# Kernel optimization log

Measured on AMD Instinct MI355X. Metric: run time of the kernel, lower is better.

## Reference

```python
import jax, jax.numpy as jnp
import numpy as np

B, T, D, H, HH, E = 32, 512, 512, 1024, 128, 4


def _ln(v, g, b, eps=1e-5):
    m = jnp.mean(v, -1, keepdims=True)
    var = jnp.mean((v - m) ** 2, -1, keepdims=True)
    return (v - m) * jax.lax.rsqrt(var + eps) * g + b


def setup_inputs() -> dict:
    key = jax.random.key(0)
    ks = jax.random.split(key, 32)
    n = lambda i, shape, s: jax.random.normal(ks[i], shape, jnp.float32) * s
    inp = {
        "x": n(0, (B, T, D), 1.0),
        # main LSTM weight, stored [in, out] = [D+H, 4H] (torch W.weight.T)
        "Wm": n(1, (D + H, 4 * H), 0.02),
        # hyper-LSTM gate weights [in, out]
        "Wi_h": n(2, (HH, HH), 0.05), "Wi_x": n(3, (D, HH), 0.02), "bi": jnp.zeros(HH),
        "Wg_h": n(4, (HH, HH), 0.05), "Wg_x": n(5, (D, HH), 0.02), "bg": jnp.zeros(HH),
        "Wf_h": n(6, (HH, HH), 0.05), "Wf_x": n(7, (D, HH), 0.02), "bf": jnp.zeros(HH),
        "Wo_h": n(8, (HH, HH), 0.05), "Wo_x": n(9, (D, HH), 0.02), "bo": jnp.zeros(HH),
        # hyper layernorm params
        "lni_g": jnp.ones(HH), "lni_b": jnp.zeros(HH),
        "lng_g": jnp.ones(HH), "lng_b": jnp.zeros(HH),
        "lnf_g": jnp.ones(HH), "lnf_b": jnp.zeros(HH),
        "lno_g": jnp.ones(HH), "lno_b": jnp.zeros(HH),
        "lnc_g": jnp.ones(HH), "lnc_b": jnp.zeros(HH),
        # z projections: [HH, 4E] + bias [4E]
        "pzx_w": n(10, (HH, 4 * E), 0.05), "pzx_b": jnp.zeros(4 * E),
        "pzh_w": n(11, (HH, 4 * E), 0.05), "pzh_b": jnp.zeros(4 * E),
        "pzb_w": n(12, (HH, 4 * E), 0.05), "pzb_b": jnp.zeros(4 * E),
        # d projections: [E, H]; bias projection has its own bias [H]
        "pdx_w": n(13, (E, H), 0.1),
        "pdh_w": n(14, (E, H), 0.1),
        "pb_w": n(15, (E, H), 0.1), "pb_b": jnp.zeros(H),
    }
    return inp


def reference(x, Wm, Wi_h, Wi_x, bi, Wg_h, Wg_x, bg, Wf_h, Wf_x, bf,
              Wo_h, Wo_x, bo, lni_g, lni_b, lng_g, lng_b, lnf_g, lnf_b,
              lno_g, lno_b, lnc_g, lnc_b, pzx_w, pzx_b, pzh_w, pzh_b,
              pzb_w, pzb_b, pdx_w, pdh_w, pb_w, pb_b):
    def step(carry, x_t):
        h, c, hh, ch = carry
        # hyper LSTM cell (with layernorms on pre-activations)
        it = jax.nn.sigmoid(_ln(hh @ Wi_h + x_t @ Wi_x + bi, lni_g, lni_b))
        gt = jnp.tanh(_ln(hh @ Wg_h + x_t @ Wg_x + bg, lng_g, lng_b))
        ft = jax.nn.sigmoid(_ln(hh @ Wf_h + x_t @ Wf_x + bf, lnf_g, lnf_b))
        ot = jax.nn.sigmoid(_ln(hh @ Wo_h + x_t @ Wo_x + bo, lno_g, lno_b))
        ch_new = ft * ch + it * gt
        hh_new = ot * jnp.tanh(_ln(ch_new, lnc_g, lnc_b))
        # embedding vectors z (chunked into 4 gates) -> per-gate scale vectors
        zx = (hh_new @ pzx_w + pzx_b).reshape(-1, 4, E)
        zh = (hh_new @ pzh_w + pzh_b).reshape(-1, 4, E)
        zb = (hh_new @ pzb_w + pzb_b).reshape(-1, 4, E)
        dx = jnp.einsum('bke,eh->bkh', zx, pdx_w).reshape(-1, 4 * H)
        dh = jnp.einsum('bke,eh->bkh', zh, pdh_w).reshape(-1, 4 * H)
        bd = (jnp.einsum('bke,eh->bkh', zb, pb_w) + pb_b).reshape(-1, 4 * H)
        # main LSTM with hyper-scaled gates
        W_x = x_t @ Wm[:D]   # [B, 4H]
        W_h = h @ Wm[D:]     # [B, 4H]
        gates = W_x * dx + W_h * dh + bd
        i, f, o, g = jnp.split(gates, 4, axis=-1)
        c_new = jax.nn.sigmoid(f) * c + jax.nn.sigmoid(i) * jnp.tanh(g)
        h_new = jax.nn.sigmoid(o) * jnp.tanh(c_new)
        return (h_new, c_new, hh_new, ch_new), h_new

    init = (jnp.zeros((B, H), x.dtype), jnp.zeros((B, H), x.dtype),
            jnp.zeros((B, HH), x.dtype), jnp.zeros((B, HH), x.dtype))
    xs = jnp.swapaxes(x, 0, 1)  # [T, B, D]
    (h, c, _, _), ys = jax.lax.scan(step, init, xs)
    outputs = jnp.swapaxes(ys, 0, 1)  # [B, T, H]
    return outputs, h, c
```

## Files before the change

kernel.cpp:

```cpp
#include <hip/hip_runtime.h>
#include <cstdint>
#include <cstddef>

#define NB 32
#define NT 512
#define ND 512
#define NH 1024
#define NC4 4608

typedef short sh8 __attribute__((ext_vector_type(8)));
typedef float f4  __attribute__((ext_vector_type(4)));
typedef unsigned int u4 __attribute__((ext_vector_type(4)));

__device__ __forceinline__ unsigned short f2bf(float x) {
  union { float f; unsigned u; } v; v.f = x;
  unsigned r = v.u + 0x7FFFu + ((v.u >> 16) & 1u);
  return (unsigned short)(r >> 16);
}
__device__ __forceinline__ float bf2f(unsigned short b) {
  union { unsigned u; float f; } v; v.u = ((unsigned)b) << 16; return v.f;
}
__device__ __forceinline__ float blo(unsigned w) { union { unsigned u; float f; } v; v.u = w << 16; return v.f; }
__device__ __forceinline__ float bhi(unsigned w) { union { unsigned u; float f; } v; v.u = w & 0xFFFF0000u; return v.f; }

#define LD16(dst, base, OFFSTR)                                         \
  asm volatile("global_load_dwordx4 %0, %1, off offset:" OFFSTR " sc0 sc1" \
               : "=v"(dst) : "v"(base))

__global__ __launch_bounds__(256) void k_prep(
    const float* __restrict__ wih, const float* __restrict__ wgh,
    const float* __restrict__ wfh, const float* __restrict__ woh,
    const float* __restrict__ pzx, const float* __restrict__ pzh,
    const float* __restrict__ pzb,
    unsigned short* __restrict__ whht, float* __restrict__ pzt,
    unsigned int* __restrict__ hbuf32, int* __restrict__ flags)
{
  int idx = blockIdx.x * 256 + threadIdx.x;
  if (idx < 65536) {
    int g = idx >> 14, r = idx & 16383, j = r >> 7, k = r & 127;
    const float* w = (g == 0) ? wih : (g == 1) ? wgh : (g == 2) ? wfh : woh;
    whht[idx] = f2bf(w[k * 128 + j]);
  }
  if (idx < 6144) {
    int r = idx & 2047, c = r >> 7, k = r & 127;
    int kind = idx >> 11;
    const float* p = (kind == 0) ? pzx : (kind == 1) ? pzh : pzb;
    pzt[idx] = p[k * 16 + c];
    (void)c; (void)k;
  }
  if (idx < 16384)
    __hip_atomic_store(hbuf32 + idx, 0u, __ATOMIC_RELAXED, __HIP_MEMORY_SCOPE_AGENT);
  if (idx < 96)
    __hip_atomic_store(flags + idx, 0, __ATOMIC_RELAXED, __HIP_MEMORY_SCOPE_AGENT);
}

__global__ __launch_bounds__(256) void k_twcat(
    const float* __restrict__ wm, const float* __restrict__ wix,
    const float* __restrict__ wgx, const float* __restrict__ wfx,
    const float* __restrict__ wox, unsigned short* __restrict__ dst)
{
  __shared__ float tile[32][33];
  int bx = blockIdx.x % 144, by = blockIdx.x / 144;
  int n0 = bx * 32, k0 = by * 32;
  int tx = threadIdx.x & 31, ty = threadIdx.x >> 5;
  #pragma unroll
  for (int i = 0; i < 4; i++) {
    int k = k0 + ty + i * 8, n = n0 + tx;
    float v;
    if (n < 4096) v = wm[(size_t)k * 4096 + n];
    else {
      int nn = n - 4096, g = nn >> 7, j = nn & 127;
      const float* w = (g == 0) ? wix : (g == 1) ? wgx : (g == 2) ? wfx : wox;
      v = w[k * 128 + j];
    }
    tile[ty + i * 8][tx] = v;
  }
  __syncthreads();
  #pragma unroll
  for (int i = 0; i < 4; i++)
    dst[(size_t)(n0 + ty + i * 8) * 512 + k0 + tx] = f2bf(tile[tx][ty + i * 8]);
}

__global__ __launch_bounds__(256) void k_twmh(
    const float* __restrict__ wm, unsigned short* __restrict__ dst)
{
  __shared__ float tile[32][33];
  int bx = blockIdx.x % 128, by = blockIdx.x / 128;
  int n0 = bx * 32, k0 = by * 32;
  int tx = threadIdx.x & 31, ty = threadIdx.x >> 5;
  #pragma unroll
  for (int i = 0; i < 4; i++)
    tile[ty + i * 8][tx] = wm[(size_t)(512 + k0 + ty + i * 8) * 4096 + n0 + tx];
  __syncthreads();
  #pragma unroll
  for (int i = 0; i < 4; i++)
    dst[(size_t)(n0 + ty + i * 8) * 1024 + k0 + tx] = f2bf(tile[tx][ty + i * 8]);
}

__global__ __launch_bounds__(256) void k_gemm(
    const float* __restrict__ x, const unsigned short* __restrict__ wt,
    unsigned short* __restrict__ preall)
{
  __shared__ unsigned short la[4096];
  __shared__ unsigned short lb[4096];
  int bid = blockIdx.x;
  int mb = bid % 128, nb = bid / 128;
  int m0 = mb * 128, n0 = nb * 128;
  int tid = threadIdx.x;
  int lane = tid & 63, wid = tid >> 6;
  int wr = (wid >> 1) * 64, wc = (wid & 1) * 64;
  f4 acc[4][4] = {};
  for (int kt = 0; kt < 16; kt++) {
    int k0 = kt * 32;
    __syncthreads();
    {
      int r = tid >> 1, kh = (tid & 1) * 16;
      const float4* srcA = (const float4*)(x + (size_t)(m0 + r) * 512 + k0 + kh);
      unsigned pk[8];
      #pragma unroll
      for (int q = 0; q < 4; q++) {
        float4 f = srcA[q];
        pk[q * 2]     = (unsigned)f2bf(f.x) | ((unsigned)f2bf(f.y) << 16);
        pk[q * 2 + 1] = (unsigned)f2bf(f.z) | ((unsigned)f2bf(f.w) << 16);
      }
      int base = r * 64 + kh * 2;
      u4 v0 = {pk[0], pk[1], pk[2], pk[3]}, v1 = {pk[4], pk[5], pk[6], pk[7]};
      *(u4*)((char*)la + ((base)      ^ ((r & 7) << 4))) = v0;
      *(u4*)((char*)la + ((base + 16) ^ ((r & 7) << 4))) = v1;
    }
    {
      int r = tid >> 1, kh = (tid & 1) * 16;
      const u4* srcB = (const u4*)(wt + (size_t)(n0 + r) * 512 + k0 + kh);
      u4 v0 = srcB[0], v1 = srcB[1];
      int base = r * 64 + kh * 2;
      *(u4*)((char*)lb + ((base)      ^ ((r & 7) << 4))) = v0;
      *(u4*)((char*)lb + ((base + 16) ^ ((r & 7) << 4))) = v1;
    }
    __syncthreads();
    int fo = (lane >> 4) * 16;
    sh8 af[4], bfr[4];
    #pragma unroll
    for (int mt = 0; mt < 4; mt++) {
      int r = wr + mt * 16 + (lane & 15);
      af[mt] = *(sh8*)((char*)la + ((r * 64 + fo) ^ ((r & 7) << 4)));
    }
    #pragma unroll
    for (int nt = 0; nt < 4; nt++) {
      int r = wc + nt * 16 + (lane & 15);
      bfr[nt] = *(sh8*)((char*)lb + ((r * 64 + fo) ^ ((r & 7) << 4)));
    }
    #pragma unroll
    for (int mt = 0; mt < 4; mt++)
      #pragma unroll
      for (int nt = 0; nt < 4; nt++)
        acc[mt][nt] = __builtin_amdgcn_mfma_f32_16x16x32_bf16(af[mt], bfr[nt], acc[mt][nt], 0, 0, 0);
  }
  #pragma unroll
  for (int mt = 0; mt < 4; mt++)
    #pragma unroll
    for (int nt = 0; nt < 4; nt++) {
      f4 a = acc[mt][nt];
      #pragma unroll
      for (int rr = 0; rr < 4; rr++) {
        int m = m0 + wr + mt * 16 + (lane >> 4) * 4 + rr;
        int n = n0 + wc + nt * 16 + (lane & 15);
        int b = m >> 9, t = m & 511;
        int nn;
        if (n < 4096) { int g = n >> 10, jh = n & 1023; nn = (jh >> 4) * 64 + g * 16 + (jh & 15); }
        else nn = n;
        preall[(size_t)(t * 32 + b) * NC4 + nn] = f2bf(a[rr]);
      }
    }
}

__global__ __launch_bounds__(256, 1) void k_rec(
    const unsigned short* __restrict__ preall,
    const unsigned short* __restrict__ wmht,
    const unsigned short* __restrict__ whht,
    const float* __restrict__ pzt,
    float* __restrict__ zbuf,
    const float* __restrict__ pdx, const float* __restrict__ pdh,
    const float* __restrict__ pbw, const float* __restrict__ pbb,
    const float* __restrict__ bi, const float* __restrict__ bg,
    const float* __restrict__ bff, const float* __restrict__ bo,
    const float* __restrict__ lnig, const float* __restrict__ lnib,
    const float* __restrict__ lngg, const float* __restrict__ lngb,
    const float* __restrict__ lnfg, const float* __restrict__ lnfb,
    const float* __restrict__ lnog, const float* __restrict__ lnob,
    const float* __restrict__ lncg, const float* __restrict__ lncb,
    const float* __restrict__ pzxb, const float* __restrict__ pzhb,
    const float* __restrict__ pzbb,
    unsigned int* __restrict__ hbuf32,
    float* __restrict__ out,
    int* __restrict__ flags)
{
  __shared__ __align__(16) unsigned short wlds[64 * 1024];
  __shared__ float red[2][32][68];
  __shared__ __align__(16) float zl[32 * 48];
  __shared__ float clds[512];
  __shared__ __align__(16) unsigned wxl[32][32];
  __shared__ float pdl[3][4][16];
  __shared__ float pbbl[16];

  const int tid = threadIdx.x;
  const int lane = tid & 63, wid = tid >> 6;

  if (blockIdx.x >= 64) {
    float* const hyp  = (float*)wlds;
    float* const pzl  = hyp;
    float* const hhs  = hyp + 6400;
    float* const chs  = hyp + 6528;
    float* const actl = hyp + 6656;
    float* const rwav = hyp + 7168;
    float* const redc = hyp + 7184;

    const int b = blockIdx.x - 64;
    const int j = tid & 127, gp = tid >> 7;
    const int ga = gp, gb = gp + 2;

    u4 wa[16], wb[16];
    {
      const u4* s = (const u4*)(whht + (size_t)(ga * 128 + j) * 128);
      #pragma unroll
      for (int i = 0; i < 16; i++) wa[i] = s[i];
      const u4* s2 = (const u4*)(whht + (size_t)(gb * 128 + j) * 128);
      #pragma unroll
      for (int i = 0; i < 16; i++) wb[i] = s2[i];
    }
    for (int i = tid; i < 6144; i += 256)
      pzl[(i >> 7) * 132 + (i & 127)] = pzt[i];

    const float* bias_p[4] = {bi, bg, bff, bo};
    const float* lng_p[4]  = {lnig, lngg, lnfg, lnog};
    const float* lnb_p[4]  = {lnib, lngb, lnfb, lnob};
    float bias_a = bias_p[ga][j], bias_b = bias_p[gb][j];
    float lgam_a = lng_p[ga][j],  lbet_a = lnb_p[ga][j];
    float lgam_b = lng_p[gb][j],  lbet_b = lnb_p[gb][j];
    float lcg = 0.f, lcb = 0.f;
    if (tid < 128) { lcg = lncg[j]; lcb = lncb[j]; hhs[j] = 0.f; chs[j] = 0.f; }
    float zbias = 0.f;
    if (tid < 48) {
      int kind = tid >> 4, c = tid & 15;
      zbias = ((kind == 0) ? pzxb : (kind == 1) ? pzhb : pzbb)[c];
    }
    __syncthreads();

    const f4* h4 = (const f4*)hhs;
    for (int t = 0; t < NT; t++) {
      float xa = bf2f(preall[(size_t)(t * 32 + b) * NC4 + 4096 + ga * 128 + j]);
      float xb = bf2f(preall[(size_t)(t * 32 + b) * NC4 + 4096 + gb * 128 + j]);
      float sa = bias_a, sb = bias_b;
      #pragma unroll
      for (int i = 0; i < 16; i++) {
        f4 h0 = h4[2 * i], h1 = h4[2 * i + 1];
        u4 w = wa[i];
        sa += blo(w.x) * h0[0] + bhi(w.x) * h0[1] + blo(w.y) * h0[2] + bhi(w.y) * h0[3]
            + blo(w.z) * h1[0] + bhi(w.z) * h1[1] + blo(w.w) * h1[2] + bhi(w.w) * h1[3];
        w = wb[i];
        sb += blo(w.x) * h0[0] + bhi(w.x) * h0[1] + blo(w.y) * h0[2] + bhi(w.y) * h0[3]
            + blo(w.z) * h1[0] + bhi(w.z) * h1[1] + blo(w.w) * h1[2] + bhi(w.w) * h1[3];
      }
      sa += xa; sb += xb;
      float a1 = sa, a2 = sa * sa, b1 = sb, b2 = sb * sb;
      #pragma unroll
      for (int m = 1; m < 64; m <<= 1) {
        a1 += __shfl_xor(a1, m); a2 += __shfl_xor(a2, m);
        b1 += __shfl_xor(b1, m); b2 += __shfl_xor(b2, m);
      }
      if ((tid & 63) == 0) {
        int w = tid >> 6;
        rwav[w * 4] = a1; rwav[w * 4 + 1] = a2; rwav[w * 4 + 2] = b1; rwav[w * 4 + 3] = b2;
      }
      __syncthreads();
      int w0 = gp * 2, w1 = gp * 2 + 1;
      float sum_a = rwav[w0 * 4] + rwav[w1 * 4],         sq_a = rwav[w0 * 4 + 1] + rwav[w1 * 4 + 1];
      float sum_b = rwav[w0 * 4 + 2] + rwav[w1 * 4 + 2], sq_b = rwav[w0 * 4 + 3] + rwav[w1 * 4 + 3];
      float mean_a = sum_a * 0.0078125f, var_a = sq_a * 0.0078125f - mean_a * mean_a;
      float mean_b = sum_b * 0.0078125f, var_b = sq_b * 0.0078125f - mean_b * mean_b;
      float xn_a = (sa - mean_a) * rsqrtf(var_a + 1e-5f) * lgam_a + lbet_a;
      float xn_b = (sb - mean_b) * rsqrtf(var_b + 1e-5f) * lgam_b + lbet_b;
      float act_a = (ga == 1) ? tanhf(xn_a) : 1.f / (1.f + __expf(-xn_a));
      float act_b = 1.f / (1.f + __expf(-xn_b));
      actl[ga * 128 + j] = act_a;
      actl[gb * 128 + j] = act_b;
      __syncthreads();
      if (tid < 128) {
        float cn = actl[2 * 128 + j] * chs[j] + actl[j] * actl[128 + j];
        chs[j] = cn;
        float c1 = cn, c2 = cn * cn;
        #pragma unroll
        for (int m = 1; m < 64; m <<= 1) { c1 += __shfl_xor(c1, m); c2 += __shfl_xor(c2, m); }
        if ((tid & 63) == 0) { int w = tid >> 6; redc[w * 2] = c1; redc[w * 2 + 1] = c2; }
      }
      __syncthreads();
      if (tid < 128) {
        float sum2 = redc[0] + redc[2], sq2 = redc[1] + redc[3];
        float mean2 = sum2 * 0.0078125f, var2 = sq2 * 0.0078125f - mean2 * mean2;
        hhs[j] = actl[3 * 128 + j] * tanhf((chs[j] - mean2) * rsqrtf(var2 + 1e-5f) * lcg + lcb);
      }
      __syncthreads();
      if (tid < 48) {
        const f4* pr = (const f4*)(pzl + tid * 132);
        float zv = zbias;
        #pragma unroll 8
        for (int q = 0; q < 32; q++) {
          f4 p = pr[q], hv = h4[q];
          zv += p[0] * hv[0] + p[1] * hv[1] + p[2] * hv[2] + p[3] * hv[3];
        }
        union { float f; unsigned u; } cv; cv.f = zv;
        __hip_atomic_store((unsigned*)zbuf + (size_t)(t * 32 + b) * 48 + tid, cv.u,
                           __ATOMIC_RELAXED, __HIP_MEMORY_SCOPE_AGENT);
      }
      asm volatile("s_waitcnt vmcnt(0)" ::: "memory");
      __syncthreads();
      if (tid == 0)
        __hip_atomic_store(flags + 64 + b, t + 1, __ATOMIC_RELAXED,
                           __HIP_MEMORY_SCOPE_AGENT);
    }
    return;
  }

  const int jh0 = blockIdx.x * 16;
  const int jw0 = blockIdx.x * 8;

  {
    int n = tid >> 2, kc = (tid & 3) * 256;
    int g = n >> 4, jo = n & 15;
    const unsigned short* src = wmht + (size_t)(g * NH + jh0 + jo) * NH + kc;
    #pragma unroll
    for (int i = 0; i < 32; i++) {
      sh8 v = *(const sh8*)(src + i * 8);
      int byte = n * 2048 + (kc + i * 8) * 2;
      *(sh8*)((char*)wlds + (byte ^ ((n & 7) << 4))) = v;
    }
  }
  clds[tid] = 0.f; clds[tid + 256] = 0.f;
  if (tid < 192) {
    int kind = tid >> 6, e = (tid >> 4) & 3, jo = tid & 15;
    const float* p = (kind == 0) ? pdx : (kind == 1) ? pdh : pbw;
    pdl[kind][e][jo] = p[e * NH + jh0 + jo];
  }
  if (tid < 16) pbbl[tid] = pbb[jh0 + tid];
  __syncthreads();

  const int bq = tid >> 3;
  const int joB = (tid & 7) * 2;
  const int kh = wid >> 1;
  const int rh = wid & 1;
  const int col = lane & 15;
  const int grp = lane >> 4;
  const int row = rh * 16 + col;

  const int zlane = (lane >= 16 && lane < 24) ? (lane - 16) : 0;
  const int* fbh = flags + lane * 4;
  const int* fbz = flags + 64 + zlane * 4;

  for (int t = 0; t < NT; t++) {
    {
      const u4* s = (const u4*)(preall + (size_t)(t * 32 + bq) * NC4
                                + (size_t)blockIdx.x * 64 + (tid & 7) * 8);
      *(u4*)&wxl[bq][(tid & 7) * 4] = *s;
    }
    if (wid == 0) {
      for (;;) {
        u4 f, g;
        if (lane < 16)      LD16(f, fbh, "0");
        else if (lane < 24) LD16(g, fbz, "0");
        asm volatile("s_waitcnt vmcnt(0)" ::: "memory");
        int ok;
        if (lane < 16)
          ok = ((int)f.x >= t) & ((int)f.y >= t) & ((int)f.z >= t) & ((int)f.w >= t);
        else if (lane < 24)
          ok = ((int)g.x > t) & ((int)g.y > t) & ((int)g.z > t) & ((int)g.w > t);
        else ok = 1;
        if (__all(ok)) break;
      }
    }
    __syncthreads();
    asm volatile("" ::: "memory");
    if (tid < 192) {
      const f4* zs = (const f4*)(zbuf + (size_t)t * NB * 48) + tid * 2;
      f4 a = zs[0], bz = zs[1];
      f4* zd = (f4*)zl + tid * 2;
      zd[0] = a; zd[1] = bz;
    }
    const unsigned int* hc32 = hbuf32 + (t & 1) * (NB * NH / 2);
    {
      const unsigned int* bp = hc32 + row * 512 + kh * 256 + grp * 4;
      u4 ar[16];
      LD16(ar[0],  bp, "0");    LD16(ar[1],  bp, "64");
      LD16(ar[2],  bp, "128");  LD16(ar[3],  bp, "192");
      LD16(ar[4],  bp, "256");  LD16(ar[5],  bp, "320");
      LD16(ar[6],  bp, "384");  LD16(ar[7],  bp, "448");
      LD16(ar[8],  bp, "512");  LD16(ar[9],  bp, "576");
      LD16(ar[10], bp, "640");  LD16(ar[11], bp, "704");
      LD16(ar[12], bp, "768");  LD16(ar[13], bp, "832");
      LD16(ar[14], bp, "896");  LD16(ar[15], bp, "960");
      asm volatile("s_waitcnt vmcnt(0)" ::: "memory");
      __builtin_amdgcn_sched_barrier(0);
      f4 acc0 = {0,0,0,0}, acc1 = {0,0,0,0}, acc2 = {0,0,0,0}, acc3 = {0,0,0,0};
      #pragma unroll
      for (int ks = 0; ks < 16; ks++) {
        int kb = kh * 512 + ks * 32 + grp * 8;
        union { u4 u; sh8 s; } A; A.u = ar[ks];
        int n0 = col, n1 = 16 + col, n2 = 32 + col, n3 = 48 + col;
        sh8 b0 = *(sh8*)((char*)wlds + ((n0 * 2048 + kb * 2) ^ ((n0 & 7) << 4)));
        sh8 b1 = *(sh8*)((char*)wlds + ((n1 * 2048 + kb * 2) ^ ((n1 & 7) << 4)));
        sh8 b2 = *(sh8*)((char*)wlds + ((n2 * 2048 + kb * 2) ^ ((n2 & 7) << 4)));
        sh8 b3 = *(sh8*)((char*)wlds + ((n3 * 2048 + kb * 2) ^ ((n3 & 7) << 4)));
        acc0 = __builtin_amdgcn_mfma_f32_16x16x32_bf16(A.s, b0, acc0, 0, 0, 0);
        acc1 = __builtin_amdgcn_mfma_f32_16x16x32_bf16(A.s, b1, acc1, 0, 0, 0);
        acc2 = __builtin_amdgcn_mfma_f32_16x16x32_bf16(A.s, b2, acc2, 0, 0, 0);
        acc3 = __builtin_amdgcn_mfma_f32_16x16x32_bf16(A.s, b3, acc3, 0, 0, 0);
      }
      int r0 = rh * 16 + grp * 4;
      #pragma unroll
      for (int rr = 0; rr < 4; rr++) {
        red[kh][r0 + rr][col]      = acc0[rr];
        red[kh][r0 + rr][16 + col] = acc1[rr];
        red[kh][r0 + rr][32 + col] = acc2[rr];
        red[kh][r0 + rr][48 + col] = acc3[rr];
      }
    }
    __syncthreads();
    float hn2[2], cn2[2];
    {
      const float* zb_ = zl + bq * 48;
      const unsigned short* wxp = (const unsigned short*)&wxl[bq][0];
      #pragma unroll
      for (int half = 0; half < 2; half++) {
        int jo = joB + half;
        float gv[4];
        #pragma unroll
        for (int g = 0; g < 4; g++) {
          float wh = red[0][bq][g * 16 + jo] + red[1][bq][g * 16 + jo];
          float dxv = 0.f, dhv = 0.f, bdv = pbbl[jo];
          #pragma unroll
          for (int e = 0; e < 4; e++) {
            dxv += zb_[g * 4 + e]      * pdl[0][e][jo];
            dhv += zb_[16 + g * 4 + e] * pdl[1][e][jo];
            bdv += zb_[32 + g * 4 + e] * pdl[2][e][jo];
          }
          float wxv = bf2f(wxp[g * 16 + jo]);
          gv[g] = wxv * dxv + wh * dhv + bdv;
        }
        float iv = 1.f / (1.f + __expf(-gv[0]));
        float fv = 1.f / (1.f + __expf(-gv[1]));
        float ov = 1.f / (1.f + __expf(-gv[2]));
        float gg = tanhf(gv[3]);
        int ci = bq * 16 + jo;
        float cn = fv * clds[ci] + iv * gg;
        clds[ci] = cn;
        hn2[half] = ov * tanhf(cn);
        cn2[half] = cn;
      }
      unsigned val = (unsigned)f2bf(hn2[0]) | ((unsigned)f2bf(hn2[1]) << 16);
      __hip_atomic_store(hbuf32 + ((t + 1) & 1) * (NB * NH / 2) + bq * 512 + jw0 + (joB >> 1),
                         val, __ATOMIC_RELAXED, __HIP_MEMORY_SCOPE_AGENT);
    }
    asm volatile("s_waitcnt vmcnt(0)" ::: "memory");
    __syncthreads();
    if (tid == 0)
      __hip_atomic_store(flags + blockIdx.x, t + 1, __ATOMIC_RELAXED,
                         __HIP_MEMORY_SCOPE_AGENT);
    *(float2*)&out[(size_t)(bq * NT + t) * NH + jh0 + joB] = make_float2(hn2[0], hn2[1]);
    if (t == NT - 1) {
      *(float2*)&out[(size_t)NB * NT * NH + bq * NH + jh0 + joB] = make_float2(hn2[0], hn2[1]);
      *(float2*)&out[(size_t)NB * NT * NH + NB * NH + bq * NH + jh0 + joB] = make_float2(cn2[0], cn2[1]);
    }
  }
}

extern "C" void kernel_launch(void* const* d_in, const int* in_sizes, int n_in,
                              void* d_out, int out_size, void* d_ws, size_t ws_size,
                              hipStream_t stream) {
  (void)in_sizes; (void)n_in; (void)out_size;
  const float* x    = (const float*)d_in[0];
  const float* Wm   = (const float*)d_in[1];
  const float* Wih  = (const float*)d_in[2];
  const float* Wix  = (const float*)d_in[3];
  const float* bi   = (const float*)d_in[4];
  const float* Wgh  = (const float*)d_in[5];
  const float* Wgx  = (const float*)d_in[6];
  const float* bg   = (const float*)d_in[7];
  const float* Wfh  = (const float*)d_in[8];
  const float* Wfx  = (const float*)d_in[9];
  const float* bfp  = (const float*)d_in[10];
  const float* Woh  = (const float*)d_in[11];
  const float* Wox  = (const float*)d_in[12];
  const float* bo   = (const float*)d_in[13];
  const float* lnig = (const float*)d_in[14];
  const float* lnib = (const float*)d_in[15];
  const float* lngg = (const float*)d_in[16];
  const float* lngb = (const float*)d_in[17];
  const float* lnfg = (const float*)d_in[18];
  const float* lnfb = (const float*)d_in[19];
  const float* lnog = (const float*)d_in[20];
  const float* lnob = (const float*)d_in[21];
  const float* lncg = (const float*)d_in[22];
  const float* lncb = (const float*)d_in[23];
  const float* pzxw = (const float*)d_in[24];
  const float* pzxb = (const float*)d_in[25];
  const float* pzhw = (const float*)d_in[26];
  const float* pzhb = (const float*)d_in[27];
  const float* pzbw = (const float*)d_in[28];
  const float* pzbb = (const float*)d_in[29];
  const float* pdx  = (const float*)d_in[30];
  const float* pdh  = (const float*)d_in[31];
  const float* pbw  = (const float*)d_in[32];
  const float* pbb  = (const float*)d_in[33];
  float* out = (float*)d_out;

  char* ws = (char*)d_ws;
  size_t off = 0;
  auto alloc = [&](size_t bytes) {
    char* p = ws + off; off += (bytes + 255) & ~(size_t)255; return p;
  };
  unsigned short* preall = (unsigned short*)alloc((size_t)16384 * NC4 * 2);
  unsigned short* wcat   = (unsigned short*)alloc((size_t)NC4 * 512 * 2);
  unsigned short* wmht   = (unsigned short*)alloc((size_t)4096 * 1024 * 2);
  unsigned short* whht   = (unsigned short*)alloc((size_t)4 * 128 * 128 * 2);
  float* pzt             = (float*)alloc((size_t)3 * 16 * 128 * 4);
  float* zbuf            = (float*)alloc((size_t)NT * NB * 48 * 4);
  unsigned int* hbuf32   = (unsigned int*)alloc((size_t)2 * NB * NH * 2);
  int* flags             = (int*)alloc((size_t)96 * 4);
  if (off > ws_size) return;

  k_prep<<<256, 256, 0, stream>>>(Wih, Wgh, Wfh, Woh, pzxw, pzhw, pzbw, whht, pzt, hbuf32, flags);
  k_twcat<<<2304, 256, 0, stream>>>(Wm, Wix, Wgx, Wfx, Wox, wcat);
  k_twmh<<<4096, 256, 0, stream>>>(Wm, wmht);
  k_gemm<<<4608, 256, 0, stream>>>(x, wcat, preall);
  k_rec<<<96, 256, 0, stream>>>(preall, wmht, whht, pzt, zbuf,
      pdx, pdh, pbw, pbb, bi, bg, bfp, bo,
      lnig, lnib, lngg, lngb, lnfg, lnfb, lnog, lnob, lncg, lncb,
      pzxb, pzhb, pzbb, hbuf32, out, flags);
}
```

Before: 3.325 ms.

## Use per-wave completion flags and staged load waits in recurrent kernel

Each wave now publishes its own step-completion flag (4 flags per block), so the block-wide barrier before signalling is gone. Consumers poll all 64 lanes' worth of h flags plus 8 hyper flags laid out in a new flag region. The hyper block signals from wave 0 before the barrier. The h-operand loads are consumed in stages with partial vmcnt waits, so MFMA work can start before all 16 loads arrive. This cuts per-timestep synchronisation latency on the serial critical path. In exchange there are more flags to poll, and wave-level signalling is only correct if each wave's stores cover the data its flag guards.

```diff
diff --git a/kernel.cpp b/kernel.cpp
--- a/kernel.cpp
+++ b/kernel.cpp
@@ -50,7 +50,7 @@
   }
   if (idx < 16384)
     __hip_atomic_store(hbuf32 + idx, 0u, __ATOMIC_RELAXED, __HIP_MEMORY_SCOPE_AGENT);
-  if (idx < 96)
+  if (idx < 288)
     __hip_atomic_store(flags + idx, 0, __ATOMIC_RELAXED, __HIP_MEMORY_SCOPE_AGENT);
 }
 
@@ -311,11 +311,13 @@
         __hip_atomic_store((unsigned*)zbuf + (size_t)(t * 32 + b) * 48 + tid, cv.u,
                            __ATOMIC_RELAXED, __HIP_MEMORY_SCOPE_AGENT);
       }
-      asm volatile("s_waitcnt vmcnt(0)" ::: "memory");
+      if (wid == 0) {
+        asm volatile("s_waitcnt vmcnt(0)" ::: "memory");
+        if (tid == 0)
+          __hip_atomic_store(flags + 256 + b, t + 1, __ATOMIC_RELAXED,
+                             __HIP_MEMORY_SCOPE_AGENT);
+      }
       __syncthreads();
-      if (tid == 0)
-        __hip_atomic_store(flags + 64 + b, t + 1, __ATOMIC_RELAXED,
-                           __HIP_MEMORY_SCOPE_AGENT);
     }
     return;
   }
@@ -351,9 +353,24 @@
   const int grp = lane >> 4;
   const int row = rh * 16 + col;
 
-  const int zlane = (lane >= 16 && lane < 24) ? (lane - 16) : 0;
   const int* fbh = flags + lane * 4;
-  const int* fbz = flags + 64 + zlane * 4;
+  const int* fbz = flags + 256 + ((lane < 8) ? lane : 0) * 4;
+
+#define WAITN(N) asm volatile("s_waitcnt vmcnt(" #N ")" ::: "memory"); __builtin_amdgcn_sched_barrier(0)
+#define PROCK(ks)                                                              \
+  {                                                                            \
+    int kb = kh * 512 + (ks) * 32 + grp * 8;                                   \
+    union { u4 u; sh8 s; } A; A.u = ar[ks];                                    \
+    int n0 = col, n1 = 16 + col, n2 = 32 + col, n3 = 48 + col;                 \
+    sh8 b0 = *(sh8*)((char*)wlds + ((n0 * 2048 + kb * 2) ^ ((n0 & 7) << 4)));  \
+    sh8 b1 = *(sh8*)((char*)wlds + ((n1 * 2048 + kb * 2) ^ ((n1 & 7) << 4)));  \
+    sh8 b2 = *(sh8*)((char*)wlds + ((n2 * 2048 + kb * 2) ^ ((n2 & 7) << 4)));  \
+    sh8 b3 = *(sh8*)((char*)wlds + ((n3 * 2048 + kb * 2) ^ ((n3 & 7) << 4)));  \
+    acc0 = __builtin_amdgcn_mfma_f32_16x16x32_bf16(A.s, b0, acc0, 0, 0, 0);    \
+    acc1 = __builtin_amdgcn_mfma_f32_16x16x32_bf16(A.s, b1, acc1, 0, 0, 0);    \
+    acc2 = __builtin_amdgcn_mfma_f32_16x16x32_bf16(A.s, b2, acc2, 0, 0, 0);    \
+    acc3 = __builtin_amdgcn_mfma_f32_16x16x32_bf16(A.s, b3, acc3, 0, 0, 0);    \
+  }
 
   for (int t = 0; t < NT; t++) {
     {
@@ -364,15 +381,12 @@
     if (wid == 0) {
       for (;;) {
         u4 f, g;
-        if (lane < 16)      LD16(f, fbh, "0");
-        else if (lane < 24) LD16(g, fbz, "0");
+        LD16(f, fbh, "0");
+        if (lane < 8) LD16(g, fbz, "0");
         asm volatile("s_waitcnt vmcnt(0)" ::: "memory");
-        int ok;
-        if (lane < 16)
-          ok = ((int)f.x >= t) & ((int)f.y >= t) & ((int)f.z >= t) & ((int)f.w >= t);
-        else if (lane < 24)
-          ok = ((int)g.x > t) & ((int)g.y > t) & ((int)g.z > t) & ((int)g.w > t);
-        else ok = 1;
+        int ok = ((int)f.x >= t) & ((int)f.y >= t) & ((int)f.z >= t) & ((int)f.w >= t);
+        if (lane < 8)
+          ok &= ((int)g.x > t) & ((int)g.y > t) & ((int)g.z > t) & ((int)g.w > t);
         if (__all(ok)) break;
       }
     }
@@ -396,23 +410,14 @@
       LD16(ar[10], bp, "640");  LD16(ar[11], bp, "704");
       LD16(ar[12], bp, "768");  LD16(ar[13], bp, "832");
       LD16(ar[14], bp, "896");  LD16(ar[15], bp, "960");
-      asm volatile("s_waitcnt vmcnt(0)" ::: "memory");
-      __builtin_amdgcn_sched_barrier(0);
       f4 acc0 = {0,0,0,0}, acc1 = {0,0,0,0}, acc2 = {0,0,0,0}, acc3 = {0,0,0,0};
-      #pragma unroll
-      for (int ks = 0; ks < 16; ks++) {
-        int kb = kh * 512 + ks * 32 + grp * 8;
-        union { u4 u; sh8 s; } A; A.u = ar[ks];
-        int n0 = col, n1 = 16 + col, n2 = 32 + col, n3 = 48 + col;
-        sh8 b0 = *(sh8*)((char*)wlds + ((n0 * 2048 + kb * 2) ^ ((n0 & 7) << 4)));
-        sh8 b1 = *(sh8*)((char*)wlds + ((n1 * 2048 + kb * 2) ^ ((n1 & 7) << 4)));
-        sh8 b2 = *(sh8*)((char*)wlds + ((n2 * 2048 + kb * 2) ^ ((n2 & 7) << 4)));
-        sh8 b3 = *(sh8*)((char*)wlds + ((n3 * 2048 + kb * 2) ^ ((n3 & 7) << 4)));
-        acc0 = __builtin_amdgcn_mfma_f32_16x16x32_bf16(A.s, b0, acc0, 0, 0, 0);
-        acc1 = __builtin_amdgcn_mfma_f32_16x16x32_bf16(A.s, b1, acc1, 0, 0, 0);
-        acc2 = __builtin_amdgcn_mfma_f32_16x16x32_bf16(A.s, b2, acc2, 0, 0, 0);
-        acc3 = __builtin_amdgcn_mfma_f32_16x16x32_bf16(A.s, b3, acc3, 0, 0, 0);
-      }
+      WAITN(8);
+      PROCK(0); PROCK(1); PROCK(2); PROCK(3);
+      PROCK(4); PROCK(5); PROCK(6); PROCK(7);
+      WAITN(4);
+      PROCK(8); PROCK(9); PROCK(10); PROCK(11);
+      WAITN(0);
+      PROCK(12); PROCK(13); PROCK(14); PROCK(15);
       int r0 = rh * 16 + grp * 4;
       #pragma unroll
       for (int rr = 0; rr < 4; rr++) {
@@ -459,9 +464,8 @@
                          val, __ATOMIC_RELAXED, __HIP_MEMORY_SCOPE_AGENT);
     }
     asm volatile("s_waitcnt vmcnt(0)" ::: "memory");
-    __syncthreads();
-    if (tid == 0)
-      __hip_atomic_store(flags + blockIdx.x, t + 1, __ATOMIC_RELAXED,
+    if (lane == 0)
+      __hip_atomic_store(flags + blockIdx.x * 4 + wid, t + 1, __ATOMIC_RELAXED,
                          __HIP_MEMORY_SCOPE_AGENT);
     *(float2*)&out[(size_t)(bq * NT + t) * NH + jh0 + joB] = make_float2(hn2[0], hn2[1]);
     if (t == NT - 1) {
@@ -469,6 +473,8 @@
       *(float2*)&out[(size_t)NB * NT * NH + NB * NH + bq * NH + jh0 + joB] = make_float2(cn2[0], cn2[1]);
     }
   }
+#undef WAITN
+#undef PROCK
 }
 
 extern "C" void kernel_launch(void* const* d_in, const int* in_sizes, int n_in,
@@ -523,7 +529,7 @@
   float* pzt             = (float*)alloc((size_t)3 * 16 * 128 * 4);
   float* zbuf            = (float*)alloc((size_t)NT * NB * 48 * 4);
   unsigned int* hbuf32   = (unsigned int*)alloc((size_t)2 * NB * NH * 2);
-  int* flags             = (int*)alloc((size_t)96 * 4);
+  int* flags             = (int*)alloc((size_t)288 * 4);
   if (off > ws_size) return;
 
   k_prep<<<256, 256, 0, stream>>>(Wih, Wgh, Wfh, Woh, pzxw, pzhw, pzbw, whht, pzt, hbuf32, flags);
```

After: 3.214 ms. 3.3% less time.
